# Kernel tuning notes

Hardware: AMD Instinct MI355X
Metric: run time of the kernel (lower is better)

The kernel has to match this reference:

```python
import jax, jax.numpy as jnp
import numpy as np
import math

D_MODEL = 1024
HEADS = 16
D_K = D_MODEL // HEADS
D_FF = 2048
EPS = 1e-6


def layer_norm(x, alpha, bias):
    # torch.std uses unbiased estimator (ddof=1)
    m = x.mean(axis=-1, keepdims=True)
    var = ((x - m) ** 2).sum(axis=-1, keepdims=True) / (x.shape[-1] - 1)
    return alpha * (x - m) / (jnp.sqrt(var) + EPS) + bias


def setup_inputs() -> dict:
    key = jax.random.key(0)
    ks = jax.random.split(key, 12)
    s = 1.0 / math.sqrt(D_MODEL)
    return {
        "x": jax.random.normal(ks[0], (2, 2048, D_MODEL), dtype=jnp.float32),
        "mask": jnp.ones((2, 1, 1, 2048), dtype=jnp.float32),
        "Wq": jax.random.uniform(ks[1], (D_MODEL, D_MODEL), minval=-s, maxval=s),
        "Wk": jax.random.uniform(ks[2], (D_MODEL, D_MODEL), minval=-s, maxval=s),
        "Wv": jax.random.uniform(ks[3], (D_MODEL, D_MODEL), minval=-s, maxval=s),
        "Wo": jax.random.uniform(ks[4], (D_MODEL, D_MODEL), minval=-s, maxval=s),
        "bo": jnp.zeros((D_MODEL,), dtype=jnp.float32),
        "W1": jax.random.uniform(ks[5], (D_MODEL, D_FF), minval=-s, maxval=s),
        "b1": jnp.zeros((D_FF,), dtype=jnp.float32),
        "W2": jax.random.uniform(ks[6], (D_FF, D_MODEL), minval=-1.0 / math.sqrt(D_FF), maxval=1.0 / math.sqrt(D_FF)),
        "b2": jnp.zeros((D_MODEL,), dtype=jnp.float32),
        "ln1_a": jnp.ones((D_MODEL,), dtype=jnp.float32),
        "ln1_b": jnp.zeros((D_MODEL,), dtype=jnp.float32),
        "ln2_a": jnp.ones((D_MODEL,), dtype=jnp.float32),
        "ln2_b": jnp.zeros((D_MODEL,), dtype=jnp.float32),
    }


def reference(x, mask, Wq, Wk, Wv, Wo, bo, W1, b1, W2, b2, ln1_a, ln1_b, ln2_a, ln2_b):
    B, S, _ = x.shape
    # --- attention sublayer (pre-LN) ---
    x2 = layer_norm(x, ln1_a, ln1_b)
    q = (x2 @ Wq).reshape(B, S, HEADS, D_K).transpose(0, 2, 1, 3)  # [B,H,S,dk]
    k = (x2 @ Wk).reshape(B, S, HEADS, D_K).transpose(0, 2, 1, 3)
    v = (x2 @ Wv).reshape(B, S, HEADS, D_K).transpose(0, 2, 1, 3)
    attn = jnp.einsum("bhqd,bhkd->bhqk", q, k) / math.sqrt(D_K)
    attn = attn * mask                                  # multiplicative mask
    attn = jnp.where(attn == 0.0, -jnp.inf, attn)       # masked_fill(==0, -inf)
    scores = jax.nn.softmax(attn, axis=-1)
    av = jnp.einsum("bhqk,bhkd->bhqd", scores, v)
    concat = av.transpose(0, 2, 1, 3).reshape(B, S, D_MODEL)
    x = x + (concat @ Wo + bo)
    # --- FFN sublayer (pre-LN) ---
    x2 = layer_norm(x, ln2_a, ln2_b)
    h = jax.nn.relu(x2 @ W1 + b1)
    x = x + (h @ W2 + b2)
    return x
```

## Files before the change

kernel.cpp:

```cpp
#include <hip/hip_runtime.h>
#include <hip/hip_bf16.h>

typedef unsigned short u16;
typedef __attribute__((ext_vector_type(4))) float f32x4;
typedef __attribute__((ext_vector_type(8))) short bf16x8;

#define SEQ 2048
#define DM 1024
#define DKK 64
#define NH 16
#define DFF 2048
#define TOK 4096

#define AS1 __attribute__((address_space(1)))
#define AS3 __attribute__((address_space(3)))

#define MFMA16(a, b, c) __builtin_amdgcn_mfma_f32_16x16x32_bf16((a), (b), (c), 0, 0, 0)

__device__ __forceinline__ u16 f2b(float f) {
  unsigned u = __float_as_uint(f);
  u = u + 0x7fffu + ((u >> 16) & 1u);
  return (u16)(u >> 16);
}

__device__ __forceinline__ unsigned cvtpk(float lo, float hi) {
  unsigned r;
  asm("v_cvt_pk_bf16_f32 %0, %1, %2" : "=v"(r) : "v"(lo), "v"(hi));
  return r;
}

__device__ __forceinline__ void gload_lds16(const u16* g, u16* l) {
  __builtin_amdgcn_global_load_lds((AS1 unsigned*)(size_t)g, (AS3 unsigned*)l, 16, 0, 0);
}

__global__ __launch_bounds__(256)
void transpose_all(const float* __restrict__ Wq, const float* __restrict__ Wk,
                   const float* __restrict__ Wv, const float* __restrict__ Wo,
                   const float* __restrict__ W1, const float* __restrict__ W2,
                   u16* __restrict__ Wqkt, u16* __restrict__ Wvt, u16* __restrict__ Wot,
                   u16* __restrict__ W1t, u16* __restrict__ W2t) {
  const int bid = blockIdx.x;
  const float* src;
  u16* dst;
  int K, N, lb;
  if (bid < 1024)      { src = Wq; dst = Wqkt;                 K = 1024; N = 1024; lb = bid; }
  else if (bid < 2048) { src = Wk; dst = Wqkt + (1 << 20);     K = 1024; N = 1024; lb = bid - 1024; }
  else if (bid < 3072) { src = Wv; dst = Wvt;                  K = 1024; N = 1024; lb = bid - 2048; }
  else if (bid < 4096) { src = Wo; dst = Wot;                  K = 1024; N = 1024; lb = bid - 3072; }
  else if (bid < 6144) { src = W1; dst = W1t;                  K = 1024; N = 2048; lb = bid - 4096; }
  else                 { src = W2; dst = W2t;                  K = 2048; N = 1024; lb = bid - 6144; }
  const int nx = N / 32;
  const int n0 = (lb % nx) * 32, k0 = (lb / nx) * 32;
  __shared__ float t[32][33];
  const int tx = threadIdx.x, ty = threadIdx.y;
#pragma unroll
  for (int i = 0; i < 4; i++) {
    int k = ty + i * 8;
    t[k][tx] = src[(size_t)(k0 + k) * N + n0 + tx];
  }
  __syncthreads();
#pragma unroll
  for (int i = 0; i < 4; i++) {
    int n = ty + i * 8;
    dst[(size_t)(n0 + n) * K + k0 + tx] = f2b(t[tx][n]);
  }
}

__global__ __launch_bounds__(256)
void ln_kernel(const float* __restrict__ x, const float* __restrict__ alpha,
               const float* __restrict__ beta, u16* __restrict__ out) {
  const int row = blockIdx.x;
  const float4 v = ((const float4*)(x + (size_t)row * DM))[threadIdx.x];
  float s = v.x + v.y + v.z + v.w;
  float q = v.x * v.x + v.y * v.y + v.z * v.z + v.w * v.w;
#pragma unroll
  for (int off = 1; off < 64; off <<= 1) {
    s += __shfl_xor(s, off);
    q += __shfl_xor(q, off);
  }
  __shared__ float ss[4], qq[4];
  const int wid = threadIdx.x >> 6;
  if ((threadIdx.x & 63) == 0) { ss[wid] = s; qq[wid] = q; }
  __syncthreads();
  s = ss[0] + ss[1] + ss[2] + ss[3];
  q = qq[0] + qq[1] + qq[2] + qq[3];
  const float mean = s * (1.f / DM);
  float var = (q - (float)DM * mean * mean) * (1.f / (DM - 1));
  var = fmaxf(var, 0.f);
  const float inv = 1.f / (sqrtf(var) + 1e-6f);
  const float4 a4 = ((const float4*)alpha)[threadIdx.x];
  const float4 b4 = ((const float4*)beta)[threadIdx.x];
  ushort4 o;
  o.x = f2b((v.x - mean) * inv * a4.x + b4.x);
  o.y = f2b((v.y - mean) * inv * a4.y + b4.y);
  o.z = f2b((v.z - mean) * inv * a4.z + b4.z);
  o.w = f2b((v.w - mean) * inv * a4.w + b4.w);
  ((ushort4*)(out + (size_t)row * DM))[threadIdx.x] = o;
}

template <int MODE, int BM, int BN>
__global__ __launch_bounds__(256, 4)
void gemm_bt(const u16* __restrict__ A, const u16* __restrict__ Bt,
             int M, int N, int K,
             const float* __restrict__ bias, const float* __restrict__ res,
             void* __restrict__ outp, float oscale, int nm) {
  constexpr int AccM = BM / 32;
  constexpr int AccN = BN / 32;
  constexpr int L = (BM == 128 ? 2 : 1) + (BN == 128 ? 2 : 1);
  __shared__ alignas(16) u16 As[3][BM * 32];
  __shared__ alignas(16) u16 Bs[3][BN * 32];
  const int nwg = gridDim.x;
  const int cpx = nwg >> 3;
  const int wg = (blockIdx.x & 7) * cpx + (blockIdx.x >> 3);
  const int bm = (wg % nm) * BM, bn = (wg / nm) * BN;
  const int tid = threadIdx.x;
  const int lane = tid & 63, w = tid >> 6;
  const int wm = (w >> 1) * (BM / 2), wn = (w & 1) * (BN / 2);
  const int r = lane & 15, g = lane >> 4;
  const int srow = tid >> 2, skk = (tid & 3) * 8;

  f32x4 acc[AccM][AccN];
#pragma unroll
  for (int i = 0; i < AccM; i++)
#pragma unroll
    for (int j = 0; j < AccN; j++) acc[i][j] = (f32x4){0.f, 0.f, 0.f, 0.f};

  const u16* aP = A + (size_t)(bm + srow) * K + skk;
  const u16* bP = Bt + (size_t)(bn + srow) * K + skk;

  auto stage = [&](int kt, int buf) {
    gload_lds16(aP + kt, &As[buf][0] + w * 512);
    if (BM == 128) gload_lds16(aP + (size_t)64 * K + kt, &As[buf][0] + w * 512 + 2048);
    gload_lds16(bP + kt, &Bs[buf][0] + w * 512);
    if (BN == 128) gload_lds16(bP + (size_t)64 * K + kt, &Bs[buf][0] + w * 512 + 2048);
  };
  auto waitL = [&]() {
    if constexpr (L == 4) asm volatile("s_waitcnt vmcnt(4) lgkmcnt(0)" ::: "memory");
    else if constexpr (L == 3) asm volatile("s_waitcnt vmcnt(3) lgkmcnt(0)" ::: "memory");
    else asm volatile("s_waitcnt vmcnt(2) lgkmcnt(0)" ::: "memory");
  };
  auto compute = [&](int buf) {
    bf16x8 af[AccM], bfr[AccN];
#pragma unroll
    for (int i = 0; i < AccM; i++) af[i] = *(const bf16x8*)(&As[buf][(wm + i * 16 + r) * 32 + g * 8]);
#pragma unroll
    for (int j = 0; j < AccN; j++) bfr[j] = *(const bf16x8*)(&Bs[buf][(wn + j * 16 + r) * 32 + g * 8]);
#pragma unroll
    for (int i = 0; i < AccM; i++)
#pragma unroll
      for (int j = 0; j < AccN; j++) acc[i][j] = MFMA16(af[i], bfr[j], acc[i][j]);
  };

  const int NKT = K / 32;
  stage(0, 0);
  stage(32, 1);
  waitL();
  __builtin_amdgcn_s_barrier();
  __builtin_amdgcn_sched_barrier(0);
  for (int it = 0; it < NKT - 2; ++it) {
    stage((it + 2) * 32, (it + 2) % 3);
    compute(it % 3);
    waitL();
    __builtin_amdgcn_s_barrier();
    __builtin_amdgcn_sched_barrier(0);
  }
  compute((NKT - 2) % 3);
  asm volatile("s_waitcnt vmcnt(0) lgkmcnt(0)" ::: "memory");
  __builtin_amdgcn_s_barrier();
  __builtin_amdgcn_sched_barrier(0);
  compute((NKT - 1) % 3);

#pragma unroll
  for (int i = 0; i < AccM; i++)
#pragma unroll
    for (int j = 0; j < AccN; j++)
#pragma unroll
      for (int t = 0; t < 4; t++) {
        const int mg = bm + wm + i * 16 + g * 4 + t;
        const int ng = bn + wn + j * 16 + r;
        const float v = acc[i][j][t];
        if (MODE == 0) {
          const int which = ng >> 10, col = ng & 1023;
          const int bb = mg >> 11, ssx = mg & 2047, hh = col >> 6, dd = col & 63;
          const float sc = which ? 1.f : oscale;
          ((u16*)outp)[(size_t)which * (TOK * (size_t)DM) +
                       ((size_t)(bb * NH + hh) * SEQ + ssx) * DKK + dd] = f2b(v * sc);
        } else if (MODE == 1) {
          const int hh = mg >> 6, dd = mg & 63, bb = ng >> 11, ssx = ng & 2047;
          ((u16*)outp)[((size_t)(bb * NH + hh) * DKK + dd) * SEQ + ssx] = f2b(v);
        } else if (MODE == 2) {
          ((float*)outp)[(size_t)mg * N + ng] = res[(size_t)mg * N + ng] + v + bias[ng];
        } else {
          const float hv = v + bias[ng];
          ((u16*)outp)[(size_t)mg * N + ng] = f2b(hv > 0.f ? hv : 0.f);
        }
      }
}

__global__ __launch_bounds__(256, 2)
void attn_kernel(const u16* __restrict__ Q, const u16* __restrict__ Kb,
                 const u16* __restrict__ Vt, const float* __restrict__ mask,
                 u16* __restrict__ outc) {
  const int bid = blockIdx.x;
  const int bh = (bid & 7) * 4 + ((bid >> 3) & 3);
  const int qt = bid >> 5;
  const int b = bh >> 4, h = bh & 15;
  const int tid = threadIdx.x, lane = tid & 63, w = tid >> 6;
  const int r = lane & 15, g = lane >> 4;
  const int qbase = qt * 64;
  const u16* Qp = Q + ((size_t)bh * SEQ + qbase) * DKK;
  const u16* Kp = Kb + (size_t)bh * SEQ * DKK;
  const u16* Vp = Vt + (size_t)bh * DKK * SEQ;
  const int wk0 = w * 512;
  const float* mk = mask + b * SEQ + wk0;

  bf16x8 bq0[4], bq1[4];
#pragma unroll
  for (int qf = 0; qf < 4; qf++) {
    bq0[qf] = *(const bf16x8*)(Qp + (size_t)(qf * 16 + r) * DKK + g * 8);
    bq1[qf] = *(const bf16x8*)(Qp + (size_t)(qf * 16 + r) * DKK + 32 + g * 8);
  }

  __shared__ __align__(16) char KV[4][2][8192];
  u16* const K0p = (u16*)&KV[w][0][0];
  u16* const K1p = (u16*)&KV[w][1][0];
  u16* const V0p = (u16*)&KV[w][0][4096];
  u16* const V1p = (u16*)&KV[w][1][4096];
  __shared__ float lrL[4][4][16];

  const int srow8 = lane >> 3;
  const int sgr = (lane & 7) ^ srow8;
  const u16* kS = Kp + (size_t)(wk0 + srow8) * DKK + sgr * 8;
  const u16* vS = Vp + (size_t)(lane >> 2) * SEQ + wk0 + (lane & 3) * 8;

  f32x4 o[4][4];
#pragma unroll
  for (int i = 0; i < 4; i++)
#pragma unroll
    for (int j = 0; j < 4; j++) o[i][j] = (f32x4){0.f, 0.f, 0.f, 0.f};
  float lr[4] = {0.f, 0.f, 0.f, 0.f};
  const int keyr = r & 7;

  gload_lds16(kS, K0p);
  gload_lds16(kS + (size_t)8 * DKK, K0p + 512);
  gload_lds16(kS + (size_t)16 * DKK, K0p + 1024);
  gload_lds16(kS + (size_t)24 * DKK, K0p + 1536);
  gload_lds16(vS, V0p);
  gload_lds16(vS + (size_t)16 * SEQ, V0p + 512);
  gload_lds16(vS + (size_t)32 * SEQ, V0p + 1024);
  gload_lds16(vS + (size_t)48 * SEQ, V0p + 1536);

#define ATILE(T, KP, VP, KPN, VPN, HASNEXT)                                           \
  do {                                                                                \
    const int kk = (T) * 32;                                                          \
    if (HASNEXT) {                                                                    \
      const int nk = kk + 32;                                                         \
      gload_lds16(kS + (size_t)nk * DKK, KPN);                                        \
      gload_lds16(kS + (size_t)(nk + 8) * DKK, KPN + 512);                            \
      gload_lds16(kS + (size_t)(nk + 16) * DKK, KPN + 1024);                          \
      gload_lds16(kS + (size_t)(nk + 24) * DKK, KPN + 1536);                          \
      gload_lds16(vS + nk, VPN);                                                      \
      gload_lds16(vS + (size_t)16 * SEQ + nk, VPN + 512);                             \
      gload_lds16(vS + (size_t)32 * SEQ + nk, VPN + 1024);                            \
      gload_lds16(vS + (size_t)48 * SEQ + nk, VPN + 1536);                            \
      asm volatile("s_waitcnt vmcnt(8)" ::: "memory");                                \
    } else {                                                                          \
      asm volatile("s_waitcnt vmcnt(0)" ::: "memory");                                \
    }                                                                                 \
    const bf16x8 ka0 = *(const bf16x8*)(KP + (size_t)(r)*64 + ((g ^ keyr) << 3));     \
    const bf16x8 ka1 = *(const bf16x8*)(KP + (size_t)(r)*64 + (((g + 4) ^ keyr) << 3));\
    const bf16x8 kb0 = *(const bf16x8*)(KP + (size_t)(16 + r) * 64 + ((g ^ keyr) << 3));\
    const bf16x8 kb1 = *(const bf16x8*)(KP + (size_t)(16 + r) * 64 + (((g + 4) ^ keyr) << 3));\
    f32x4 s0[4], s1[4];                                                               \
    __builtin_amdgcn_s_setprio(1);                                                    \
    _Pragma("unroll")                                                                 \
    for (int qf = 0; qf < 4; qf++) {                                                  \
      f32x4 z = (f32x4){0.f, 0.f, 0.f, 0.f};                                          \
      z = MFMA16(ka0, bq0[qf], z);                                                    \
      z = MFMA16(ka1, bq1[qf], z);                                                    \
      s0[qf] = z;                                                                     \
      f32x4 y = (f32x4){0.f, 0.f, 0.f, 0.f};                                          \
      y = MFMA16(kb0, bq0[qf], y);                                                    \
      y = MFMA16(kb1, bq1[qf], y);                                                    \
      s1[qf] = y;                                                                     \
    }                                                                                 \
    __builtin_amdgcn_s_setprio(0);                                                    \
    const float4 m0 = *(const float4*)(mk + kk + 4 * g);                              \
    const float4 m1 = *(const float4*)(mk + kk + 16 + 4 * g);                         \
    const int ones = (m0.x == 1.f) & (m0.y == 1.f) & (m0.z == 1.f) & (m0.w == 1.f) &  \
                     (m1.x == 1.f) & (m1.y == 1.f) & (m1.z == 1.f) & (m1.w == 1.f);   \
    const bool fastm = __all(ones);                                                   \
    bf16x8 pa[4];                                                                     \
    _Pragma("unroll")                                                                 \
    for (int qf = 0; qf < 4; qf++) {                                                  \
      float p[8];                                                                     \
      if (fastm) {                                                                    \
        p[0] = __builtin_amdgcn_exp2f(s0[qf][0]);                                     \
        p[1] = __builtin_amdgcn_exp2f(s0[qf][1]);                                     \
        p[2] = __builtin_amdgcn_exp2f(s0[qf][2]);                                     \
        p[3] = __builtin_amdgcn_exp2f(s0[qf][3]);                                     \
        p[4] = __builtin_amdgcn_exp2f(s1[qf][0]);                                     \
        p[5] = __builtin_amdgcn_exp2f(s1[qf][1]);                                     \
        p[6] = __builtin_amdgcn_exp2f(s1[qf][2]);                                     \
        p[7] = __builtin_amdgcn_exp2f(s1[qf][3]);                                     \
      } else {                                                                        \
        float pr;                                                                     \
        pr = s0[qf][0] * m0.x; p[0] = (pr == 0.f) ? 0.f : __builtin_amdgcn_exp2f(pr); \
        pr = s0[qf][1] * m0.y; p[1] = (pr == 0.f) ? 0.f : __builtin_amdgcn_exp2f(pr); \
        pr = s0[qf][2] * m0.z; p[2] = (pr == 0.f) ? 0.f : __builtin_amdgcn_exp2f(pr); \
        pr = s0[qf][3] * m0.w; p[3] = (pr == 0.f) ? 0.f : __builtin_amdgcn_exp2f(pr); \
        pr = s1[qf][0] * m1.x; p[4] = (pr == 0.f) ? 0.f : __builtin_amdgcn_exp2f(pr); \
        pr = s1[qf][1] * m1.y; p[5] = (pr == 0.f) ? 0.f : __builtin_amdgcn_exp2f(pr); \
        pr = s1[qf][2] * m1.z; p[6] = (pr == 0.f) ? 0.f : __builtin_amdgcn_exp2f(pr); \
        pr = s1[qf][3] * m1.w; p[7] = (pr == 0.f) ? 0.f : __builtin_amdgcn_exp2f(pr); \
      }                                                                               \
      float rs = ((p[0] + p[1]) + (p[2] + p[3])) + ((p[4] + p[5]) + (p[6] + p[7]));   \
      rs += __shfl_xor(rs, 16);                                                       \
      rs += __shfl_xor(rs, 32);                                                       \
      lr[qf] += rs;                                                                   \
      const unsigned w0 = cvtpk(p[0], p[1]), w1 = cvtpk(p[2], p[3]);                  \
      const unsigned w2 = cvtpk(p[4], p[5]), w3 = cvtpk(p[6], p[7]);                  \
      union { unsigned u[4]; bf16x8 v; } pu;                                          \
      _Pragma("unroll")                                                               \
      for (int c = 0; c < 4; c++) {                                                   \
        const int srcl = r + ((g & 1) * 2 + (c >> 1)) * 16;                           \
        const unsigned lo = __shfl((c & 1) ? w1 : w0, srcl);                          \
        const unsigned hi = __shfl((c & 1) ? w3 : w2, srcl);                          \
        pu.u[c] = (g < 2) ? lo : hi;                                                  \
      }                                                                               \
      pa[qf] = pu.v;                                                                  \
    }                                                                                 \
    __builtin_amdgcn_s_setprio(1);                                                    \
    _Pragma("unroll")                                                                 \
    for (int dc = 0; dc < 4; dc++) {                                                  \
      const bf16x8 bv = *(const bf16x8*)(VP + (size_t)(dc * 16 + r) * 32 + g * 8);    \
      _Pragma("unroll")                                                               \
      for (int qf = 0; qf < 4; qf++) o[qf][dc] = MFMA16(pa[qf], bv, o[qf][dc]);       \
    }                                                                                 \
    __builtin_amdgcn_s_setprio(0);                                                    \
  } while (0)

  for (int tt = 0; tt < 16; tt += 2) {
    ATILE(tt, K0p, V0p, K1p, V1p, true);
    ATILE(tt + 1, K1p, V1p, K0p, V0p, (tt < 14));
  }
#undef ATILE

  float* mo = (float*)&KV[0][0][0];
  float* mw = mo + w * 4096;
#pragma unroll
  for (int qf = 0; qf < 4; qf++)
#pragma unroll
    for (int dc = 0; dc < 4; dc++)
      *(f32x4*)(mw + (size_t)((qf * 4 + dc) * 64 + lane) * 4) = o[qf][dc];
  if (lane < 16) {
#pragma unroll
    for (int qf = 0; qf < 4; qf++) lrL[w][qf][lane] = lr[qf];
  }
  __syncthreads();

  const int qf = w;
  float lq[4];
#pragma unroll
  for (int t = 0; t < 4; t++)
    lq[t] = ((lrL[0][qf][4 * g + t] + lrL[1][qf][4 * g + t]) +
             (lrL[2][qf][4 * g + t] + lrL[3][qf][4 * g + t]));
#pragma unroll
  for (int dc = 0; dc < 4; dc++) {
    f32x4 a0 = *(const f32x4*)(mo + 0 * 4096 + (size_t)((qf * 4 + dc) * 64 + lane) * 4);
    f32x4 a1 = *(const f32x4*)(mo + 1 * 4096 + (size_t)((qf * 4 + dc) * 64 + lane) * 4);
    f32x4 a2 = *(const f32x4*)(mo + 2 * 4096 + (size_t)((qf * 4 + dc) * 64 + lane) * 4);
    f32x4 a3 = *(const f32x4*)(mo + 3 * 4096 + (size_t)((qf * 4 + dc) * 64 + lane) * 4);
#pragma unroll
    for (int t = 0; t < 4; t++) {
      const float val = ((a0[t] + a1[t]) + (a2[t] + a3[t])) / lq[t];
      const int srow_g = qbase + qf * 16 + g * 4 + t;
      outc[((size_t)(b * SEQ + srow_g)) * DM + h * DKK + dc * 16 + r] = f2b(val);
    }
  }
}

extern "C" void kernel_launch(void* const* d_in, const int* in_sizes, int n_in,
                              void* d_out, int out_size, void* d_ws, size_t ws_size,
                              hipStream_t stream) {
  const float* x    = (const float*)d_in[0];
  const float* mask = (const float*)d_in[1];
  const float* Wq   = (const float*)d_in[2];
  const float* Wk   = (const float*)d_in[3];
  const float* Wv   = (const float*)d_in[4];
  const float* Wo   = (const float*)d_in[5];
  const float* bo   = (const float*)d_in[6];
  const float* W1   = (const float*)d_in[7];
  const float* b1   = (const float*)d_in[8];
  const float* W2   = (const float*)d_in[9];
  const float* b2   = (const float*)d_in[10];
  const float* l1a  = (const float*)d_in[11];
  const float* l1b  = (const float*)d_in[12];
  const float* l2a  = (const float*)d_in[13];
  const float* l2b  = (const float*)d_in[14];

  char* wsb = (char*)d_ws;
  u16* Wqkt = (u16*)(wsb + (0ull << 20));
  u16* Wvt  = (u16*)(wsb + (4ull << 20));
  u16* Wot  = (u16*)(wsb + (6ull << 20));
  u16* W1t  = (u16*)(wsb + (8ull << 20));
  u16* W2t  = (u16*)(wsb + (12ull << 20));
  u16* x2   = (u16*)(wsb + (16ull << 20));
  u16* qkb  = (u16*)(wsb + (24ull << 20));
  u16* vtb  = (u16*)(wsb + (40ull << 20));
  float* x1 = (float*)(wsb + (48ull << 20));
  u16* concat = x2;
  u16* x2b = qkb;
  u16* hb  = (u16*)(wsb + (32ull << 20));

  const float qscale = 0.125f * 1.4426950408889634f;

  transpose_all<<<dim3(8192), dim3(32, 8), 0, stream>>>(Wq, Wk, Wv, Wo, W1, W2,
                                                        Wqkt, Wvt, Wot, W1t, W2t);

  ln_kernel<<<TOK, 256, 0, stream>>>(x, l1a, l1b, x2);

  gemm_bt<0, 64, 128><<<dim3(1024), 256, 0, stream>>>(
      x2, Wqkt, TOK, 2048, DM, nullptr, nullptr, qkb, qscale, 64);
  gemm_bt<1, 64, 64><<<dim3(1024), 256, 0, stream>>>(
      Wvt, x2, DM, TOK, DM, nullptr, nullptr, vtb, 1.0f, 16);

  attn_kernel<<<dim3(1024), 256, 0, stream>>>(qkb, qkb + (size_t)TOK * DM, vtb, mask, concat);

  gemm_bt<2, 64, 64><<<dim3(1024), 256, 0, stream>>>(
      concat, Wot, TOK, DM, DM, bo, x, x1, 1.0f, 64);

  ln_kernel<<<TOK, 256, 0, stream>>>(x1, l2a, l2b, x2b);

  gemm_bt<3, 64, 128><<<dim3(1024), 256, 0, stream>>>(
      x2b, W1t, TOK, DFF, DM, b1, nullptr, hb, 1.0f, 64);
  gemm_bt<2, 64, 64><<<dim3(1024), 256, 0, stream>>>(
      hb, W2t, TOK, DM, DFF, b2, x1, (float*)d_out, 1.0f, 64);
}
```

Baseline: 227.7 us.

## Shrink attention LDS footprint with register-staged V and drop GEMM block swizzle

The attention kernel now keeps K double-buffered in LDS but stages V through registers into a single LDS buffer. It also splits the final cross-wave reduction into two halves so the scratch area fits in the smaller LDS allocation. Together these let launch_bounds request 4 blocks per CU instead of 2, trading some load latency hiding on V and an extra barrier for higher occupancy. Separately, the GEMMs drop the XCD-aware 1D block remapping in favour of a plain 2D grid, which may hurt L2 locality across chiplets.

```diff
diff --git a/kernel.cpp b/kernel.cpp
--- a/kernel.cpp
+++ b/kernel.cpp
@@ -103,16 +103,13 @@
 void gemm_bt(const u16* __restrict__ A, const u16* __restrict__ Bt,
              int M, int N, int K,
              const float* __restrict__ bias, const float* __restrict__ res,
-             void* __restrict__ outp, float oscale, int nm) {
+             void* __restrict__ outp, float oscale) {
   constexpr int AccM = BM / 32;
   constexpr int AccN = BN / 32;
   constexpr int L = (BM == 128 ? 2 : 1) + (BN == 128 ? 2 : 1);
   __shared__ alignas(16) u16 As[3][BM * 32];
   __shared__ alignas(16) u16 Bs[3][BN * 32];
-  const int nwg = gridDim.x;
-  const int cpx = nwg >> 3;
-  const int wg = (blockIdx.x & 7) * cpx + (blockIdx.x >> 3);
-  const int bm = (wg % nm) * BM, bn = (wg / nm) * BN;
+  const int bm = blockIdx.x * BM, bn = blockIdx.y * BN;
   const int tid = threadIdx.x;
   const int lane = tid & 63, w = tid >> 6;
   const int wm = (w >> 1) * (BM / 2), wn = (w & 1) * (BN / 2);
@@ -197,7 +194,7 @@
       }
 }
 
-__global__ __launch_bounds__(256, 2)
+__global__ __launch_bounds__(256, 4)
 void attn_kernel(const u16* __restrict__ Q, const u16* __restrict__ Kb,
                  const u16* __restrict__ Vt, const float* __restrict__ mask,
                  u16* __restrict__ outc) {
@@ -221,17 +218,18 @@
     bq1[qf] = *(const bf16x8*)(Qp + (size_t)(qf * 16 + r) * DKK + 32 + g * 8);
   }
 
-  __shared__ __align__(16) char KV[4][2][8192];
-  u16* const K0p = (u16*)&KV[w][0][0];
-  u16* const K1p = (u16*)&KV[w][1][0];
-  u16* const V0p = (u16*)&KV[w][0][4096];
-  u16* const V1p = (u16*)&KV[w][1][4096];
+  __shared__ __align__(16) u16 Ks[4][2][32 * 64];
+  __shared__ __align__(16) u16 Vs[4][64 * 32];
   __shared__ float lrL[4][4][16];
 
   const int srow8 = lane >> 3;
   const int sgr = (lane & 7) ^ srow8;
   const u16* kS = Kp + (size_t)(wk0 + srow8) * DKK + sgr * 8;
   const u16* vS = Vp + (size_t)(lane >> 2) * SEQ + wk0 + (lane & 3) * 8;
+  u16* const Kw0 = &Ks[w][0][0];
+  u16* const Kw1 = &Ks[w][1][0];
+  u16* const Vw = &Vs[w][0];
+  u16* const vD = Vw + (lane >> 2) * 32 + (lane & 3) * 8;
 
   f32x4 o[4][4];
 #pragma unroll
@@ -241,36 +239,35 @@
   float lr[4] = {0.f, 0.f, 0.f, 0.f};
   const int keyr = r & 7;
 
-  gload_lds16(kS, K0p);
-  gload_lds16(kS + (size_t)8 * DKK, K0p + 512);
-  gload_lds16(kS + (size_t)16 * DKK, K0p + 1024);
-  gload_lds16(kS + (size_t)24 * DKK, K0p + 1536);
-  gload_lds16(vS, V0p);
-  gload_lds16(vS + (size_t)16 * SEQ, V0p + 512);
-  gload_lds16(vS + (size_t)32 * SEQ, V0p + 1024);
-  gload_lds16(vS + (size_t)48 * SEQ, V0p + 1536);
-
-#define ATILE(T, KP, VP, KPN, VPN, HASNEXT)                                           \
+  gload_lds16(kS, Kw0);
+  gload_lds16(kS + (size_t)8 * DKK, Kw0 + 512);
+  gload_lds16(kS + (size_t)16 * DKK, Kw0 + 1024);
+  gload_lds16(kS + (size_t)24 * DKK, Kw0 + 1536);
+  int4 vst0 = *(const int4*)(vS);
+  int4 vst1 = *(const int4*)(vS + (size_t)16 * SEQ);
+  int4 vst2 = *(const int4*)(vS + (size_t)32 * SEQ);
+  int4 vst3 = *(const int4*)(vS + (size_t)48 * SEQ);
+  asm volatile("s_waitcnt vmcnt(0)" ::: "memory");
+  *(int4*)(vD) = vst0;
+  *(int4*)(vD + 512) = vst1;
+  *(int4*)(vD + 1024) = vst2;
+  *(int4*)(vD + 1536) = vst3;
+  gload_lds16(kS + (size_t)32 * DKK, Kw1);
+  gload_lds16(kS + (size_t)40 * DKK, Kw1 + 512);
+  gload_lds16(kS + (size_t)48 * DKK, Kw1 + 1024);
+  gload_lds16(kS + (size_t)56 * DKK, Kw1 + 1536);
+  vst0 = *(const int4*)(vS + 32);
+  vst1 = *(const int4*)(vS + (size_t)16 * SEQ + 32);
+  vst2 = *(const int4*)(vS + (size_t)32 * SEQ + 32);
+  vst3 = *(const int4*)(vS + (size_t)48 * SEQ + 32);
+
+#define ASTEP(I, KCUR)                                                                \
   do {                                                                                \
-    const int kk = (T) * 32;                                                          \
-    if (HASNEXT) {                                                                    \
-      const int nk = kk + 32;                                                         \
-      gload_lds16(kS + (size_t)nk * DKK, KPN);                                        \
-      gload_lds16(kS + (size_t)(nk + 8) * DKK, KPN + 512);                            \
-      gload_lds16(kS + (size_t)(nk + 16) * DKK, KPN + 1024);                          \
-      gload_lds16(kS + (size_t)(nk + 24) * DKK, KPN + 1536);                          \
-      gload_lds16(vS + nk, VPN);                                                      \
-      gload_lds16(vS + (size_t)16 * SEQ + nk, VPN + 512);                             \
-      gload_lds16(vS + (size_t)32 * SEQ + nk, VPN + 1024);                            \
-      gload_lds16(vS + (size_t)48 * SEQ + nk, VPN + 1536);                            \
-      asm volatile("s_waitcnt vmcnt(8)" ::: "memory");                                \
-    } else {                                                                          \
-      asm volatile("s_waitcnt vmcnt(0)" ::: "memory");                                \
-    }                                                                                 \
-    const bf16x8 ka0 = *(const bf16x8*)(KP + (size_t)(r)*64 + ((g ^ keyr) << 3));     \
-    const bf16x8 ka1 = *(const bf16x8*)(KP + (size_t)(r)*64 + (((g + 4) ^ keyr) << 3));\
-    const bf16x8 kb0 = *(const bf16x8*)(KP + (size_t)(16 + r) * 64 + ((g ^ keyr) << 3));\
-    const bf16x8 kb1 = *(const bf16x8*)(KP + (size_t)(16 + r) * 64 + (((g + 4) ^ keyr) << 3));\
+    const int kk = (I) * 32;                                                          \
+    const bf16x8 ka0 = *(const bf16x8*)(KCUR + r * 64 + ((g ^ keyr) << 3));           \
+    const bf16x8 ka1 = *(const bf16x8*)(KCUR + r * 64 + (((g + 4) ^ keyr) << 3));     \
+    const bf16x8 kb0 = *(const bf16x8*)(KCUR + (16 + r) * 64 + ((g ^ keyr) << 3));    \
+    const bf16x8 kb1 = *(const bf16x8*)(KCUR + (16 + r) * 64 + (((g + 4) ^ keyr) << 3)); \
     f32x4 s0[4], s1[4];                                                               \
     __builtin_amdgcn_s_setprio(1);                                                    \
     _Pragma("unroll")                                                                 \
@@ -333,49 +330,96 @@
     __builtin_amdgcn_s_setprio(1);                                                    \
     _Pragma("unroll")                                                                 \
     for (int dc = 0; dc < 4; dc++) {                                                  \
-      const bf16x8 bv = *(const bf16x8*)(VP + (size_t)(dc * 16 + r) * 32 + g * 8);    \
+      const bf16x8 bv = *(const bf16x8*)(Vw + (dc * 16 + r) * 32 + g * 8);            \
       _Pragma("unroll")                                                               \
       for (int qf = 0; qf < 4; qf++) o[qf][dc] = MFMA16(pa[qf], bv, o[qf][dc]);       \
     }                                                                                 \
     __builtin_amdgcn_s_setprio(0);                                                    \
+    if ((I) < 15) {                                                                   \
+      asm volatile("s_waitcnt vmcnt(0)" ::: "memory");                                \
+      *(int4*)(vD) = vst0;                                                            \
+      *(int4*)(vD + 512) = vst1;                                                      \
+      *(int4*)(vD + 1024) = vst2;                                                     \
+      *(int4*)(vD + 1536) = vst3;                                                     \
+      if ((I) < 14) {                                                                 \
+        const int nk = kk + 64;                                                       \
+        gload_lds16(kS + (size_t)nk * DKK, KCUR);                                     \
+        gload_lds16(kS + (size_t)(nk + 8) * DKK, KCUR + 512);                         \
+        gload_lds16(kS + (size_t)(nk + 16) * DKK, KCUR + 1024);                       \
+        gload_lds16(kS + (size_t)(nk + 24) * DKK, KCUR + 1536);                       \
+        vst0 = *(const int4*)(vS + nk);                                               \
+        vst1 = *(const int4*)(vS + (size_t)16 * SEQ + nk);                            \
+        vst2 = *(const int4*)(vS + (size_t)32 * SEQ + nk);                            \
+        vst3 = *(const int4*)(vS + (size_t)48 * SEQ + nk);                            \
+      }                                                                               \
+    }                                                                                 \
   } while (0)
 
   for (int tt = 0; tt < 16; tt += 2) {
-    ATILE(tt, K0p, V0p, K1p, V1p, true);
-    ATILE(tt + 1, K1p, V1p, K0p, V0p, (tt < 14));
-  }
-#undef ATILE
-
-  float* mo = (float*)&KV[0][0][0];
-  float* mw = mo + w * 4096;
-#pragma unroll
-  for (int qf = 0; qf < 4; qf++)
+    ASTEP(tt, Kw0);
+    ASTEP(tt + 1, Kw1);
+  }
+#undef ASTEP
+
+  if (lane < 16) {
+#pragma unroll
+    for (int qf = 0; qf < 4; qf++) lrL[w][qf][lane] = lr[qf];
+  }
+  float* mo = (float*)&Ks[0][0][0];
+  float* mw = mo + w * 2048;
+#pragma unroll
+  for (int qf = 0; qf < 2; qf++)
 #pragma unroll
     for (int dc = 0; dc < 4; dc++)
       *(f32x4*)(mw + (size_t)((qf * 4 + dc) * 64 + lane) * 4) = o[qf][dc];
-  if (lane < 16) {
-#pragma unroll
-    for (int qf = 0; qf < 4; qf++) lrL[w][qf][lane] = lr[qf];
-  }
   __syncthreads();
-
-  const int qf = w;
-  float lq[4];
-#pragma unroll
-  for (int t = 0; t < 4; t++)
-    lq[t] = ((lrL[0][qf][4 * g + t] + lrL[1][qf][4 * g + t]) +
-             (lrL[2][qf][4 * g + t] + lrL[3][qf][4 * g + t]));
-#pragma unroll
-  for (int dc = 0; dc < 4; dc++) {
-    f32x4 a0 = *(const f32x4*)(mo + 0 * 4096 + (size_t)((qf * 4 + dc) * 64 + lane) * 4);
-    f32x4 a1 = *(const f32x4*)(mo + 1 * 4096 + (size_t)((qf * 4 + dc) * 64 + lane) * 4);
-    f32x4 a2 = *(const f32x4*)(mo + 2 * 4096 + (size_t)((qf * 4 + dc) * 64 + lane) * 4);
-    f32x4 a3 = *(const f32x4*)(mo + 3 * 4096 + (size_t)((qf * 4 + dc) * 64 + lane) * 4);
-#pragma unroll
-    for (int t = 0; t < 4; t++) {
-      const float val = ((a0[t] + a1[t]) + (a2[t] + a3[t])) / lq[t];
-      const int srow_g = qbase + qf * 16 + g * 4 + t;
-      outc[((size_t)(b * SEQ + srow_g)) * DM + h * DKK + dc * 16 + r] = f2b(val);
+  if (w < 2) {
+    const int qf = w;
+    float lq[4];
+#pragma unroll
+    for (int t = 0; t < 4; t++)
+      lq[t] = ((lrL[0][qf][4 * g + t] + lrL[1][qf][4 * g + t]) +
+               (lrL[2][qf][4 * g + t] + lrL[3][qf][4 * g + t]));
+#pragma unroll
+    for (int dc = 0; dc < 4; dc++) {
+      f32x4 a0 = *(const f32x4*)(mo + 0 * 2048 + (size_t)((qf * 4 + dc) * 64 + lane) * 4);
+      f32x4 a1 = *(const f32x4*)(mo + 1 * 2048 + (size_t)((qf * 4 + dc) * 64 + lane) * 4);
+      f32x4 a2 = *(const f32x4*)(mo + 2 * 2048 + (size_t)((qf * 4 + dc) * 64 + lane) * 4);
+      f32x4 a3 = *(const f32x4*)(mo + 3 * 2048 + (size_t)((qf * 4 + dc) * 64 + lane) * 4);
+#pragma unroll
+      for (int t = 0; t < 4; t++) {
+        const float val = ((a0[t] + a1[t]) + (a2[t] + a3[t])) / lq[t];
+        const int srow_g = qbase + qf * 16 + g * 4 + t;
+        outc[((size_t)(b * SEQ + srow_g)) * DM + h * DKK + dc * 16 + r] = f2b(val);
+      }
+    }
+  }
+  __syncthreads();
+#pragma unroll
+  for (int qf = 2; qf < 4; qf++)
+#pragma unroll
+    for (int dc = 0; dc < 4; dc++)
+      *(f32x4*)(mw + (size_t)(((qf - 2) * 4 + dc) * 64 + lane) * 4) = o[qf][dc];
+  __syncthreads();
+  if (w >= 2) {
+    const int qf = w;
+    float lq[4];
+#pragma unroll
+    for (int t = 0; t < 4; t++)
+      lq[t] = ((lrL[0][qf][4 * g + t] + lrL[1][qf][4 * g + t]) +
+               (lrL[2][qf][4 * g + t] + lrL[3][qf][4 * g + t]));
+#pragma unroll
+    for (int dc = 0; dc < 4; dc++) {
+      f32x4 a0 = *(const f32x4*)(mo + 0 * 2048 + (size_t)(((qf - 2) * 4 + dc) * 64 + lane) * 4);
+      f32x4 a1 = *(const f32x4*)(mo + 1 * 2048 + (size_t)(((qf - 2) * 4 + dc) * 64 + lane) * 4);
+      f32x4 a2 = *(const f32x4*)(mo + 2 * 2048 + (size_t)(((qf - 2) * 4 + dc) * 64 + lane) * 4);
+      f32x4 a3 = *(const f32x4*)(mo + 3 * 2048 + (size_t)(((qf - 2) * 4 + dc) * 64 + lane) * 4);
+#pragma unroll
+      for (int t = 0; t < 4; t++) {
+        const float val = ((a0[t] + a1[t]) + (a2[t] + a3[t])) / lq[t];
+        const int srow_g = qbase + qf * 16 + g * 4 + t;
+        outc[((size_t)(b * SEQ + srow_g)) * DM + h * DKK + dc * 16 + r] = f2b(val);
+      }
     }
   }
 }
@@ -420,20 +464,20 @@
 
   ln_kernel<<<TOK, 256, 0, stream>>>(x, l1a, l1b, x2);
 
-  gemm_bt<0, 64, 128><<<dim3(1024), 256, 0, stream>>>(
-      x2, Wqkt, TOK, 2048, DM, nullptr, nullptr, qkb, qscale, 64);
-  gemm_bt<1, 64, 64><<<dim3(1024), 256, 0, stream>>>(
-      Wvt, x2, DM, TOK, DM, nullptr, nullptr, vtb, 1.0f, 16);
+  gemm_bt<0, 64, 128><<<dim3(TOK / 64, 2048 / 128), 256, 0, stream>>>(
+      x2, Wqkt, TOK, 2048, DM, nullptr, nullptr, qkb, qscale);
+  gemm_bt<1, 64, 64><<<dim3(DM / 64, TOK / 64), 256, 0, stream>>>(
+      Wvt, x2, DM, TOK, DM, nullptr, nullptr, vtb, 1.0f);
 
   attn_kernel<<<dim3(1024), 256, 0, stream>>>(qkb, qkb + (size_t)TOK * DM, vtb, mask, concat);
 
-  gemm_bt<2, 64, 64><<<dim3(1024), 256, 0, stream>>>(
-      concat, Wot, TOK, DM, DM, bo, x, x1, 1.0f, 64);
+  gemm_bt<2, 64, 64><<<dim3(TOK / 64, DM / 64), 256, 0, stream>>>(
+      concat, Wot, TOK, DM, DM, bo, x, x1, 1.0f);
 
   ln_kernel<<<TOK, 256, 0, stream>>>(x1, l2a, l2b, x2b);
 
-  gemm_bt<3, 64, 128><<<dim3(1024), 256, 0, stream>>>(
-      x2b, W1t, TOK, DFF, DM, b1, nullptr, hb, 1.0f, 64);
-  gemm_bt<2, 64, 64><<<dim3(1024), 256, 0, stream>>>(
-      hb, W2t, TOK, DM, DFF, b2, x1, (float*)d_out, 1.0f, 64);
-}
+  gemm_bt<3, 64, 128><<<dim3(TOK / 64, DFF / 128), 256, 0, stream>>>(
+      x2b, W1t, TOK, DFF, DM, b1, nullptr, hb, 1.0f);
+  gemm_bt<2, 64, 64><<<dim3(TOK / 64, DM / 64), 256, 0, stream>>>(
+      hb, W2t, TOK, DM, DFF, b2, x1, (float*)d_out, 1.0f);
+}
```

Measured after the change: 266.5 us. 17.0% more time.
